# Performance work log

Hardware: AMD Instinct MI355X
Metric: run time of the kernel (lower is better)

## Reference

```python
import jax, jax.numpy as jnp
import numpy as np
from jax import lax

B, C, L = 32, 8, 4096
K, S = 128, 64  # num_shapelets, shapelets_size


def setup_inputs() -> dict:
    key = jax.random.key(0)
    kx, ks = jax.random.split(key)
    x = jax.random.normal(kx, (B, C, L), dtype=jnp.float32)
    shapelets = jax.random.normal(ks, (C, K, S), dtype=jnp.float32)
    return {"x": x, "shapelets": shapelets}


def reference(x, shapelets):
    # x: (B, C, L); shapelets: (C, K, S)
    # Equivalent to: unfold -> cdist(p=2) -> sum over channels -> min over windows.
    # Use the ||a-b||^2 = ||a||^2 + ||b||^2 - 2 a.b expansion so the unfolded
    # (B, C, W, S) tensor is never materialized; cross-terms via grouped conv.
    Bc, Cc, Lc = x.shape
    _, Kc, Sc = shapelets.shape
    dn = ("NCH", "OIH", "NCH")
    # cross[b, c*K+k, w] = sum_s x[b,c,w+s] * shapelets[c,k,s]
    rhs = shapelets.reshape(Cc * Kc, 1, Sc)
    cross = lax.conv_general_dilated(x, rhs, (1,), "VALID",
                                     feature_group_count=Cc,
                                     dimension_numbers=dn)  # (B, C*K, W)
    W = cross.shape[-1]
    cross = cross.reshape(Bc, Cc, Kc, W)
    # sliding window squared norms of x: conv of x^2 with ones kernel per channel
    ones = jnp.ones((Cc, 1, Sc), x.dtype)
    xnorm = lax.conv_general_dilated(x * x, ones, (1,), "VALID",
                                     feature_group_count=Cc,
                                     dimension_numbers=dn)  # (B, C, W)
    snorm = jnp.sum(shapelets * shapelets, axis=-1)  # (C, K)
    d2 = xnorm[:, :, None, :] + snorm[None, :, :, None] - 2.0 * cross  # (B,C,K,W)
    d = jnp.sqrt(jnp.maximum(d2, 1e-12))
    summed = jnp.sum(d, axis=1, keepdims=True)  # (B, 1, K, W)
    return jnp.min(summed, axis=3)  # (B, 1, K)
```

## Files before the change

kernel.cpp:

```cpp
#include <hip/hip_runtime.h>


typedef short short8 __attribute__((ext_vector_type(8)));
typedef float f32x4 __attribute__((ext_vector_type(4)));

constexpr int Bn = 32, Cn = 8, Ln = 4096, Kn = 128, Sn = 64;
constexpr int Wn = Ln - Sn + 1;
constexpr int WT = 128;
constexpr int NWT = (Wn + WT - 1) / WT;
constexpr int BDIM = 256;

__device__ __forceinline__ unsigned int f2bf(float f) {
  unsigned int u = __float_as_uint(f);
  u += 0x7FFFu + ((u >> 16) & 1u);
  return u >> 16;
}

__global__ void prep_kernel(const float* __restrict__ sh,
                            unsigned int* __restrict__ out,
                            unsigned short* __restrict__ hbf,
                            float* __restrict__ snorm) {
  int gid = blockIdx.x * blockDim.x + threadIdx.x;
  out[gid] = 0x7F7FFFFFu;
  if (gid < Cn * Kn) {
    const float4* row = (const float4*)(sh + (size_t)gid * Sn);
    uint2* orow = (uint2*)(hbf + (size_t)gid * Sn);
    float a = 0.f;
    #pragma unroll
    for (int i = 0; i < 16; ++i) {
      float4 v = row[i];
      a += v.x * v.x + v.y * v.y + v.z * v.z + v.w * v.w;
      unsigned int p0 = f2bf(-2.f * v.x) | (f2bf(-2.f * v.y) << 16);
      unsigned int p1 = f2bf(-2.f * v.z) | (f2bf(-2.f * v.w) << 16);
      orow[i] = make_uint2(p0, p1);
    }
    snorm[gid] = a;
  }
}

__launch_bounds__(BDIM, 2)
__global__ void med_kernel(const float* __restrict__ x,
                           const unsigned short* __restrict__ hbf,
                           const float* __restrict__ snorm,
                           unsigned int* __restrict__ out) {
  constexpr int XRS = 200;
  constexpr int BSS = 80;
  __shared__ __align__(16) unsigned short Xr[8 * XRS];
  __shared__ __align__(16) unsigned short Bs[Kn * BSS];
  __shared__ __align__(16) float xnormC[Cn * WT];
  __shared__ __align__(16) float snormC[Cn * Kn];

  const int tid  = threadIdx.x;
  const int b    = blockIdx.y;
  const int w0   = blockIdx.x * WT;
  const int lane = tid & 63;
  const int wv   = tid >> 6;
  const int quad = lane >> 4;
  const int n16  = lane & 15;
  const int wbase = wv * 32;

  const float* xb = x + (size_t)b * Cn * Ln;

  ((float4*)snormC)[tid] = ((const float4*)snorm)[tid];

  {
    int c  = tid >> 5;
    int m0 = (tid & 31) * 4;
    const float* xc = xb + c * Ln;
    auto xq = [&](int i) -> float {
      float v = (i < Ln) ? xc[i] : 0.f;
      return v * v;
    };
    float s0 = 0.f;
    for (int s = 0; s < Sn; ++s) s0 += xq(w0 + m0 + s);
    float s1 = s0 - xq(w0 + m0 + 0) + xq(w0 + m0 + 64);
    float s2 = s1 - xq(w0 + m0 + 1) + xq(w0 + m0 + 65);
    float s3 = s2 - xq(w0 + m0 + 2) + xq(w0 + m0 + 66);
    xnormC[c * WT + m0 + 0] = s0;
    xnormC[c * WT + m0 + 1] = s1;
    xnormC[c * WT + m0 + 2] = s2;
    xnormC[c * WT + m0 + 3] = s3;
  }

  float dist[2][8][4] = {};

  for (int c = 0; c < Cn; ++c) {
    __syncthreads();

    {
      const float* xc = xb + c * Ln;
      #pragma unroll
      for (int rep = 0; rep < 3; ++rep) {
        int pid = tid + rep * BDIM;
        int r = pid / 96;
        int p = pid - r * 96;
        int i0 = w0 + r + 2 * p;
        float f0 = (i0 < Ln) ? xc[i0] : 0.f;
        float f1 = (i0 + 1 < Ln) ? xc[i0 + 1] : 0.f;
        *(unsigned int*)(&Xr[r * XRS + 2 * p]) = f2bf(f0) | (f2bf(f1) << 16);
      }
    }
    {
      const uint4* hb = (const uint4*)(hbf + (size_t)c * Kn * Sn);
      #pragma unroll
      for (int rep = 0; rep < 4; ++rep) {
        int qid = tid + rep * BDIM;
        int k = qid >> 3, ch = qid & 7;
        *(uint4*)(&Bs[k * BSS + ch * 8]) = hb[qid];
      }
    }
    __syncthreads();

    float4 xn[2];
    #pragma unroll
    for (int mt = 0; mt < 2; ++mt)
      xn[mt] = *(const float4*)(&xnormC[c * WT + wbase + mt * 16 + quad * 4]);

    short8 af[2][2];
    #pragma unroll
    for (int mt = 0; mt < 2; ++mt)
      #pragma unroll
      for (int ks = 0; ks < 2; ++ks) {
        int i = wbase + mt * 16 + n16 + ks * 32 + quad * 8;
        af[mt][ks] = *(const short8*)(&Xr[(i & 7) * XRS + (i >> 3) * 8]);
      }

    #pragma unroll
    for (int pass = 0; pass < 2; ++pass) {
      short8 bfr[4][2];
      float sn[4];
      #pragma unroll
      for (int nt = 0; nt < 4; ++nt) {
        int ksh = pass * 64 + nt * 16 + n16;
        sn[nt] = snormC[c * Kn + ksh];
        #pragma unroll
        for (int ks = 0; ks < 2; ++ks)
          bfr[nt][ks] = *(const short8*)(&Bs[ksh * BSS + ks * 32 + quad * 8]);
      }
      #pragma unroll
      for (int mt = 0; mt < 2; ++mt)
        #pragma unroll
        for (int nt = 0; nt < 4; ++nt) {
          f32x4 acc;
          #pragma unroll
          for (int rg = 0; rg < 4; ++rg) acc[rg] = xn[mt][rg] + sn[nt];
          acc = __builtin_amdgcn_mfma_f32_16x16x32_bf16(af[mt][0], bfr[nt][0], acc, 0, 0, 0);
          acc = __builtin_amdgcn_mfma_f32_16x16x32_bf16(af[mt][1], bfr[nt][1], acc, 0, 0, 0);
          #pragma unroll
          for (int rg = 0; rg < 4; ++rg)
            dist[mt][pass * 4 + nt][rg] += __builtin_amdgcn_sqrtf(acc[rg]);
        }
    }
  }

  const int wql = w0 + wbase + quad * 4;
  #pragma unroll
  for (int nt2 = 0; nt2 < 8; ++nt2) {
    float v = 3.4e38f;
    #pragma unroll
    for (int mt = 0; mt < 2; ++mt)
      #pragma unroll
      for (int rg = 0; rg < 4; ++rg) {
        int wg = wql + mt * 16 + rg;
        float d = (wg < Wn) ? dist[mt][nt2][rg] : 3.4e38f;
        v = fminf(v, d);
      }
    v = fminf(v, __shfl_xor(v, 16, 64));
    v = fminf(v, __shfl_xor(v, 32, 64));
    if (lane < 16)
      atomicMin(&out[b * Kn + nt2 * 16 + n16], __float_as_uint(v));
  }
}

extern "C" void kernel_launch(void* const* d_in, const int* in_sizes, int n_in,
                              void* d_out, int out_size, void* d_ws, size_t ws_size,
                              hipStream_t stream) {
  const float* x  = (const float*)d_in[0];
  const float* sh = (const float*)d_in[1];
  unsigned int* out = (unsigned int*)d_out;
  unsigned short* hbf = (unsigned short*)d_ws;
  float* snorm = (float*)((char*)d_ws + (size_t)Cn * Kn * Sn * 2);
  hipLaunchKernelGGL(prep_kernel, dim3(16), dim3(256), 0, stream, sh, out, hbf, snorm);
  hipLaunchKernelGGL(med_kernel, dim3(NWT, Bn), dim3(BDIM), 0, stream, x, hbf, snorm, out);
}
```

Baseline: 112.8 us.

## Double-buffer channel staging with async global-to-LDS loads and XOR-swizzled B

Double-buffers the per-channel x tile and shapelet tile in shared memory. The next channel's data is prefetched while the current channel's MFMAs run: shapelets are copied directly global-to-LDS via global_load_lds, and x values are held in registers and written after compute. The shapelet layout is XOR-swizzled in the prep kernel so the unpadded LDS rows avoid bank conflicts, and launch bounds ask for 3 blocks per SM. The aim is to hide load latency and cut one barrier per channel, at the cost of more LDS and register pressure.

```diff
diff --git a/kernel.cpp b/kernel.cpp
--- a/kernel.cpp
+++ b/kernel.cpp
@@ -9,6 +9,9 @@
 constexpr int WT = 128;
 constexpr int NWT = (Wn + WT - 1) / WT;
 constexpr int BDIM = 256;
+
+typedef const __attribute__((address_space(1))) unsigned int gas_u32;
+typedef __attribute__((address_space(3))) unsigned int las_u32;
 
 __device__ __forceinline__ unsigned int f2bf(float f) {
   unsigned int u = __float_as_uint(f);
@@ -24,7 +27,8 @@
   out[gid] = 0x7F7FFFFFu;
   if (gid < Cn * Kn) {
     const float4* row = (const float4*)(sh + (size_t)gid * Sn);
-    uint2* orow = (uint2*)(hbf + (size_t)gid * Sn);
+    char* rowb = (char*)hbf + (size_t)gid * (Sn * 2);
+    const unsigned int sw = (gid & 7u) << 4;
     float a = 0.f;
     #pragma unroll
     for (int i = 0; i < 16; ++i) {
@@ -32,21 +36,20 @@
       a += v.x * v.x + v.y * v.y + v.z * v.z + v.w * v.w;
       unsigned int p0 = f2bf(-2.f * v.x) | (f2bf(-2.f * v.y) << 16);
       unsigned int p1 = f2bf(-2.f * v.z) | (f2bf(-2.f * v.w) << 16);
-      orow[i] = make_uint2(p0, p1);
+      *(uint2*)(rowb + ((8u * i) ^ sw)) = make_uint2(p0, p1);
     }
     snorm[gid] = a;
   }
 }
 
-__launch_bounds__(BDIM, 2)
+__launch_bounds__(BDIM, 3)
 __global__ void med_kernel(const float* __restrict__ x,
                            const unsigned short* __restrict__ hbf,
                            const float* __restrict__ snorm,
                            unsigned int* __restrict__ out) {
   constexpr int XRS = 200;
-  constexpr int BSS = 80;
-  __shared__ __align__(16) unsigned short Xr[8 * XRS];
-  __shared__ __align__(16) unsigned short Bs[Kn * BSS];
+  __shared__ __align__(16) unsigned short Xr[2][8 * XRS];
+  __shared__ __align__(16) unsigned short Bs[2][Kn * Sn];
   __shared__ __align__(16) float xnormC[Cn * WT];
   __shared__ __align__(16) float snormC[Cn * Kn];
 
@@ -61,7 +64,47 @@
 
   const float* xb = x + (size_t)b * Cn * Ln;
 
+  auto stage_b = [&](int bufi, int c) {
+    const char* src = (const char*)hbf + (size_t)c * (Kn * Sn * 2);
+    char* dst = (char*)&Bs[bufi][0];
+    #pragma unroll
+    for (int rep = 0; rep < 4; ++rep) {
+      int q16 = (tid + rep * BDIM) * 16;
+      __builtin_amdgcn_global_load_lds((gas_u32*)(src + q16), (las_u32*)(dst + q16),
+                                       16, 0, 0);
+    }
+  };
+
+  int x_lds[3], x_g[3];
+  #pragma unroll
+  for (int rep = 0; rep < 3; ++rep) {
+    int pid = tid + rep * BDIM;
+    int r = pid / 96;
+    int p = pid - r * 96;
+    x_lds[rep] = r * XRS + 2 * p;
+    x_g[rep] = w0 + r + 2 * p;
+  }
+  float xf[3][2];
+  auto load_x = [&](int c) {
+    const float* xc = xb + (size_t)c * Ln;
+    #pragma unroll
+    for (int rep = 0; rep < 3; ++rep) {
+      int i0 = x_g[rep];
+      xf[rep][0] = (i0 < Ln) ? xc[i0] : 0.f;
+      xf[rep][1] = (i0 + 1 < Ln) ? xc[i0 + 1] : 0.f;
+    }
+  };
+  auto write_x = [&](int bufi) {
+    #pragma unroll
+    for (int rep = 0; rep < 3; ++rep)
+      *(unsigned int*)(&Xr[bufi][x_lds[rep]]) =
+          f2bf(xf[rep][0]) | (f2bf(xf[rep][1]) << 16);
+  };
+
   ((float4*)snormC)[tid] = ((const float4*)snorm)[tid];
+
+  stage_b(0, 0);
+  load_x(0);
 
   {
     int c  = tid >> 5;
@@ -81,35 +124,18 @@
     xnormC[c * WT + m0 + 2] = s2;
     xnormC[c * WT + m0 + 3] = s3;
   }
+  write_x(0);
+  __syncthreads();
 
   float dist[2][8][4] = {};
 
   for (int c = 0; c < Cn; ++c) {
-    __syncthreads();
-
-    {
-      const float* xc = xb + c * Ln;
-      #pragma unroll
-      for (int rep = 0; rep < 3; ++rep) {
-        int pid = tid + rep * BDIM;
-        int r = pid / 96;
-        int p = pid - r * 96;
-        int i0 = w0 + r + 2 * p;
-        float f0 = (i0 < Ln) ? xc[i0] : 0.f;
-        float f1 = (i0 + 1 < Ln) ? xc[i0 + 1] : 0.f;
-        *(unsigned int*)(&Xr[r * XRS + 2 * p]) = f2bf(f0) | (f2bf(f1) << 16);
-      }
-    }
-    {
-      const uint4* hb = (const uint4*)(hbf + (size_t)c * Kn * Sn);
-      #pragma unroll
-      for (int rep = 0; rep < 4; ++rep) {
-        int qid = tid + rep * BDIM;
-        int k = qid >> 3, ch = qid & 7;
-        *(uint4*)(&Bs[k * BSS + ch * 8]) = hb[qid];
-      }
-    }
-    __syncthreads();
+    const int buf = c & 1;
+
+    if (c + 1 < Cn) {
+      stage_b(buf ^ 1, c + 1);
+      load_x(c + 1);
+    }
 
     float4 xn[2];
     #pragma unroll
@@ -122,9 +148,10 @@
       #pragma unroll
       for (int ks = 0; ks < 2; ++ks) {
         int i = wbase + mt * 16 + n16 + ks * 32 + quad * 8;
-        af[mt][ks] = *(const short8*)(&Xr[(i & 7) * XRS + (i >> 3) * 8]);
+        af[mt][ks] = *(const short8*)(&Xr[buf][(i & 7) * XRS + (i >> 3) * 8]);
       }
 
+    const char* bsb = (const char*)&Bs[buf][0];
     #pragma unroll
     for (int pass = 0; pass < 2; ++pass) {
       short8 bfr[4][2];
@@ -134,8 +161,10 @@
         int ksh = pass * 64 + nt * 16 + n16;
         sn[nt] = snormC[c * Kn + ksh];
         #pragma unroll
-        for (int ks = 0; ks < 2; ++ks)
-          bfr[nt][ks] = *(const short8*)(&Bs[ksh * BSS + ks * 32 + quad * 8]);
+        for (int ks = 0; ks < 2; ++ks) {
+          int off = (ksh * 128 + ks * 64 + quad * 16) ^ ((ksh & 7) << 4);
+          bfr[nt][ks] = *(const short8*)(bsb + off);
+        }
       }
       #pragma unroll
       for (int mt = 0; mt < 2; ++mt)
@@ -151,6 +180,9 @@
             dist[mt][pass * 4 + nt][rg] += __builtin_amdgcn_sqrtf(acc[rg]);
         }
     }
+
+    if (c + 1 < Cn) write_x(buf ^ 1);
+    __syncthreads();
   }
 
   const int wql = w0 + wbase + quad * 4;
```

Measured after the change: 205.3 us. 1.82x slower.

## Stage all channels of x in LDS once and read shapelets directly from global

Applied to the files above, without the earlier changes.

The kernel now converts the x tile for all eight channels to bf16 in shared memory up front, with a single barrier, instead of reloading per channel between two barriers. Shapelet B-fragments and norms are loaded straight from global/L2 into registers, which removes the Bs and snormC staging. The K dimension is split into two halves of 64 in a non-unrolled outer loop, so the dist accumulators shrink and register pressure drops. The tradeoffs are redundant global loads of shapelets, since every wave reads them, and shapelet loads that are no longer amortised through LDS.

```diff
diff --git a/kernel.cpp b/kernel.cpp
--- a/kernel.cpp
+++ b/kernel.cpp
@@ -44,11 +44,8 @@
                            const float* __restrict__ snorm,
                            unsigned int* __restrict__ out) {
   constexpr int XRS = 200;
-  constexpr int BSS = 80;
-  __shared__ __align__(16) unsigned short Xr[8 * XRS];
-  __shared__ __align__(16) unsigned short Bs[Kn * BSS];
+  __shared__ __align__(16) unsigned short Xr[Cn][8 * XRS];
   __shared__ __align__(16) float xnormC[Cn * WT];
-  __shared__ __align__(16) float snormC[Cn * Kn];
 
   const int tid  = threadIdx.x;
   const int b    = blockIdx.y;
@@ -61,7 +58,32 @@
 
   const float* xb = x + (size_t)b * Cn * Ln;
 
-  ((float4*)snormC)[tid] = ((const float4*)snorm)[tid];
+  int x_lds[3], x_g[3];
+  #pragma unroll
+  for (int rep = 0; rep < 3; ++rep) {
+    int pid = tid + rep * BDIM;
+    int r = pid / 96;
+    int p = pid - r * 96;
+    x_lds[rep] = r * XRS + 2 * p;
+    x_g[rep] = w0 + r + 2 * p;
+  }
+  const bool safe = (w0 + 198 <= Ln);
+  #pragma unroll 1
+  for (int c = 0; c < Cn; ++c) {
+    const float* xc = xb + (size_t)c * Ln;
+    #pragma unroll
+    for (int rep = 0; rep < 3; ++rep) {
+      float f0, f1;
+      if (safe) {
+        f0 = xc[x_g[rep]];
+        f1 = xc[x_g[rep] + 1];
+      } else {
+        f0 = (x_g[rep] < Ln) ? xc[x_g[rep]] : 0.f;
+        f1 = (x_g[rep] + 1 < Ln) ? xc[x_g[rep] + 1] : 0.f;
+      }
+      *(unsigned int*)(&Xr[c][x_lds[rep]]) = f2bf(f0) | (f2bf(f1) << 16);
+    }
+  }
 
   {
     int c  = tid >> 5;
@@ -71,8 +93,14 @@
       float v = (i < Ln) ? xc[i] : 0.f;
       return v * v;
     };
-    float s0 = 0.f;
-    for (int s = 0; s < Sn; ++s) s0 += xq(w0 + m0 + s);
+    float a0 = 0.f, a1 = 0.f, a2 = 0.f, a3 = 0.f;
+    for (int s = 0; s < Sn; s += 4) {
+      a0 += xq(w0 + m0 + s);
+      a1 += xq(w0 + m0 + s + 1);
+      a2 += xq(w0 + m0 + s + 2);
+      a3 += xq(w0 + m0 + s + 3);
+    }
+    float s0 = (a0 + a1) + (a2 + a3);
     float s1 = s0 - xq(w0 + m0 + 0) + xq(w0 + m0 + 64);
     float s2 = s1 - xq(w0 + m0 + 1) + xq(w0 + m0 + 65);
     float s3 = s2 - xq(w0 + m0 + 2) + xq(w0 + m0 + 66);
@@ -81,94 +109,68 @@
     xnormC[c * WT + m0 + 2] = s2;
     xnormC[c * WT + m0 + 3] = s3;
   }
+  __syncthreads();
 
-  float dist[2][8][4] = {};
+  const int wql = w0 + wbase + quad * 4;
+  const char* hbase = (const char*)hbf + n16 * 128 + quad * 16;
 
-  for (int c = 0; c < Cn; ++c) {
-    __syncthreads();
+  #pragma unroll 1
+  for (int gh = 0; gh < 2; ++gh) {
+    float dist[4][2][4] = {};
 
-    {
-      const float* xc = xb + c * Ln;
-      #pragma unroll
-      for (int rep = 0; rep < 3; ++rep) {
-        int pid = tid + rep * BDIM;
-        int r = pid / 96;
-        int p = pid - r * 96;
-        int i0 = w0 + r + 2 * p;
-        float f0 = (i0 < Ln) ? xc[i0] : 0.f;
-        float f1 = (i0 + 1 < Ln) ? xc[i0 + 1] : 0.f;
-        *(unsigned int*)(&Xr[r * XRS + 2 * p]) = f2bf(f0) | (f2bf(f1) << 16);
-      }
-    }
-    {
-      const uint4* hb = (const uint4*)(hbf + (size_t)c * Kn * Sn);
-      #pragma unroll
-      for (int rep = 0; rep < 4; ++rep) {
-        int qid = tid + rep * BDIM;
-        int k = qid >> 3, ch = qid & 7;
-        *(uint4*)(&Bs[k * BSS + ch * 8]) = hb[qid];
-      }
-    }
-    __syncthreads();
-
-    float4 xn[2];
-    #pragma unroll
-    for (int mt = 0; mt < 2; ++mt)
-      xn[mt] = *(const float4*)(&xnormC[c * WT + wbase + mt * 16 + quad * 4]);
-
-    short8 af[2][2];
-    #pragma unroll
-    for (int mt = 0; mt < 2; ++mt)
-      #pragma unroll
-      for (int ks = 0; ks < 2; ++ks) {
-        int i = wbase + mt * 16 + n16 + ks * 32 + quad * 8;
-        af[mt][ks] = *(const short8*)(&Xr[(i & 7) * XRS + (i >> 3) * 8]);
-      }
-
-    #pragma unroll
-    for (int pass = 0; pass < 2; ++pass) {
-      short8 bfr[4][2];
-      float sn[4];
-      #pragma unroll
-      for (int nt = 0; nt < 4; ++nt) {
-        int ksh = pass * 64 + nt * 16 + n16;
-        sn[nt] = snormC[c * Kn + ksh];
-        #pragma unroll
-        for (int ks = 0; ks < 2; ++ks)
-          bfr[nt][ks] = *(const short8*)(&Bs[ksh * BSS + ks * 32 + quad * 8]);
-      }
+    #pragma unroll 1
+    for (int c = 0; c < Cn; ++c) {
+      short8 af[2][2];
       #pragma unroll
       for (int mt = 0; mt < 2; ++mt)
         #pragma unroll
-        for (int nt = 0; nt < 4; ++nt) {
+        for (int ks = 0; ks < 2; ++ks) {
+          int i = wbase + mt * 16 + n16 + ks * 32 + quad * 8;
+          af[mt][ks] = *(const short8*)(&Xr[c][(i & 7) * XRS + (i >> 3) * 8]);
+        }
+      float4 xn[2];
+      #pragma unroll
+      for (int mt = 0; mt < 2; ++mt)
+        xn[mt] = *(const float4*)(&xnormC[c * WT + wbase + mt * 16 + quad * 4]);
+
+      const char* hc = hbase + (c * Kn + gh * 64) * (Sn * 2);
+      const float* snc = snorm + c * Kn + gh * 64 + n16;
+
+      #pragma unroll
+      for (int gl = 0; gl < 4; ++gl) {
+        short8 b0 = *(const short8*)(hc + gl * 2048);
+        short8 b1 = *(const short8*)(hc + gl * 2048 + 64);
+        float sn = snc[gl * 16];
+        #pragma unroll
+        for (int mt = 0; mt < 2; ++mt) {
           f32x4 acc;
           #pragma unroll
-          for (int rg = 0; rg < 4; ++rg) acc[rg] = xn[mt][rg] + sn[nt];
-          acc = __builtin_amdgcn_mfma_f32_16x16x32_bf16(af[mt][0], bfr[nt][0], acc, 0, 0, 0);
-          acc = __builtin_amdgcn_mfma_f32_16x16x32_bf16(af[mt][1], bfr[nt][1], acc, 0, 0, 0);
+          for (int rg = 0; rg < 4; ++rg) acc[rg] = xn[mt][rg] + sn;
+          acc = __builtin_amdgcn_mfma_f32_16x16x32_bf16(af[mt][0], b0, acc, 0, 0, 0);
+          acc = __builtin_amdgcn_mfma_f32_16x16x32_bf16(af[mt][1], b1, acc, 0, 0, 0);
           #pragma unroll
           for (int rg = 0; rg < 4; ++rg)
-            dist[mt][pass * 4 + nt][rg] += __builtin_amdgcn_sqrtf(acc[rg]);
+            dist[gl][mt][rg] += __builtin_amdgcn_sqrtf(acc[rg]);
         }
+      }
     }
-  }
 
-  const int wql = w0 + wbase + quad * 4;
-  #pragma unroll
-  for (int nt2 = 0; nt2 < 8; ++nt2) {
-    float v = 3.4e38f;
     #pragma unroll
-    for (int mt = 0; mt < 2; ++mt)
+    for (int gl = 0; gl < 4; ++gl) {
+      float v = 3.4e38f;
       #pragma unroll
-      for (int rg = 0; rg < 4; ++rg) {
-        int wg = wql + mt * 16 + rg;
-        float d = (wg < Wn) ? dist[mt][nt2][rg] : 3.4e38f;
-        v = fminf(v, d);
-      }
-    v = fminf(v, __shfl_xor(v, 16, 64));
-    v = fminf(v, __shfl_xor(v, 32, 64));
-    if (lane < 16)
-      atomicMin(&out[b * Kn + nt2 * 16 + n16], __float_as_uint(v));
+      for (int mt = 0; mt < 2; ++mt)
+        #pragma unroll
+        for (int rg = 0; rg < 4; ++rg) {
+          int wg = wql + mt * 16 + rg;
+          float d = (wg < Wn) ? dist[gl][mt][rg] : 3.4e38f;
+          v = fminf(v, d);
+        }
+      v = fminf(v, __shfl_xor(v, 16, 64));
+      v = fminf(v, __shfl_xor(v, 32, 64));
+      if (lane < 16)
+        atomicMin(&out[b * Kn + (gh * 4 + gl) * 16 + n16], __float_as_uint(v));
+    }
   }
 }
 
```

Result: slower. 141.3 us (+25.2%).

## Split shapelets across waves, double-buffer per-wave LDS staging, drop block barriers

Applied to the files above, without the earlier changes.

Each wave now owns a 32-shapelet slice across all 128 windows instead of a 32-window slice across all shapelets, so every wave stages its own B tile (via global_load_lds into XOR-swizzled LDS) and its own copy of the bf16 window tile. This removes the per-channel __syncthreads and lets the next channel's loads be issued before the current channel's MFMAs, a double-buffered software pipeline. The cost is that each wave redundantly converts and stores the whole X tile, which means more global loads and LDS traffic. LDS use also grows, which may lower occupancy.

```diff
diff --git a/kernel.cpp b/kernel.cpp
--- a/kernel.cpp
+++ b/kernel.cpp
@@ -9,6 +9,12 @@
 constexpr int WT = 128;
 constexpr int NWT = (Wn + WT - 1) / WT;
 constexpr int BDIM = 256;
+constexpr int XRS = 200;
+constexpr int PPR = 96;
+constexpr int PAIRS = 8 * PPR;
+
+typedef const __attribute__((address_space(1))) unsigned int gas_u32;
+typedef __attribute__((address_space(3))) unsigned int las_u32;
 
 __device__ __forceinline__ unsigned int f2bf(float f) {
   unsigned int u = __float_as_uint(f);
@@ -24,7 +30,8 @@
   out[gid] = 0x7F7FFFFFu;
   if (gid < Cn * Kn) {
     const float4* row = (const float4*)(sh + (size_t)gid * Sn);
-    uint2* orow = (uint2*)(hbf + (size_t)gid * Sn);
+    char* rowb = (char*)hbf + (size_t)gid * (Sn * 2);
+    const unsigned int sw = (gid & 7u) << 4;
     float a = 0.f;
     #pragma unroll
     for (int i = 0; i < 16; ++i) {
@@ -32,7 +39,7 @@
       a += v.x * v.x + v.y * v.y + v.z * v.z + v.w * v.w;
       unsigned int p0 = f2bf(-2.f * v.x) | (f2bf(-2.f * v.y) << 16);
       unsigned int p1 = f2bf(-2.f * v.z) | (f2bf(-2.f * v.w) << 16);
-      orow[i] = make_uint2(p0, p1);
+      *(uint2*)(rowb + ((8u * i) ^ sw)) = make_uint2(p0, p1);
     }
     snorm[gid] = a;
   }
@@ -43,10 +50,8 @@
                            const unsigned short* __restrict__ hbf,
                            const float* __restrict__ snorm,
                            unsigned int* __restrict__ out) {
-  constexpr int XRS = 200;
-  constexpr int BSS = 80;
-  __shared__ __align__(16) unsigned short Xr[8 * XRS];
-  __shared__ __align__(16) unsigned short Bs[Kn * BSS];
+  __shared__ __align__(16) unsigned short Xr[4][2][8 * XRS];
+  __shared__ __align__(16) unsigned short Bs[4][32 * Sn];
   __shared__ __align__(16) float xnormC[Cn * WT];
   __shared__ __align__(16) float snormC[Cn * Kn];
 
@@ -57,11 +62,48 @@
   const int wv   = tid >> 6;
   const int quad = lane >> 4;
   const int n16  = lane & 15;
-  const int wbase = wv * 32;
+  const int kq   = wv;
 
   const float* xb = x + (size_t)b * Cn * Ln;
 
+  auto stage_b = [&](int c) {
+    const char* src = (const char*)hbf + ((size_t)c * Kn + kq * 32) * (Sn * 2);
+    char* dst = (char*)&Bs[wv][0];
+    #pragma unroll
+    for (int rep = 0; rep < 4; ++rep) {
+      int q16 = lane * 16 + rep * 1024;
+      __builtin_amdgcn_global_load_lds((gas_u32*)(src + q16), (las_u32*)(dst + q16),
+                                       16, 0, 0);
+    }
+  };
+
+  auto stage_x = [&](int c, int xbuf) {
+    const float* xc = xb + (size_t)c * Ln;
+    #pragma unroll
+    for (int bt = 0; bt < 3; ++bt) {
+      float a[4][2];
+      #pragma unroll
+      for (int sub = 0; sub < 4; ++sub) {
+        int pid = lane + (bt * 4 + sub) * 64;
+        int r = pid / PPR, p = pid - r * PPR;
+        int i0 = w0 + r + 2 * p;
+        a[sub][0] = (i0 < Ln) ? xc[i0] : 0.f;
+        a[sub][1] = (i0 + 1 < Ln) ? xc[i0 + 1] : 0.f;
+      }
+      #pragma unroll
+      for (int sub = 0; sub < 4; ++sub) {
+        int pid = lane + (bt * 4 + sub) * 64;
+        int r = pid / PPR, p = pid - r * PPR;
+        *(unsigned int*)(&Xr[wv][xbuf][r * XRS + 2 * p]) =
+            f2bf(a[sub][0]) | (f2bf(a[sub][1]) << 16);
+      }
+    }
+  };
+
   ((float4*)snormC)[tid] = ((const float4*)snorm)[tid];
+
+  stage_b(0);
+  stage_x(0, 0);
 
   {
     int c  = tid >> 5;
@@ -81,94 +123,70 @@
     xnormC[c * WT + m0 + 2] = s2;
     xnormC[c * WT + m0 + 3] = s3;
   }
-
-  float dist[2][8][4] = {};
+  __syncthreads();
+
+  float dist[8][2][4] = {};
+  int buf = 0;
 
   for (int c = 0; c < Cn; ++c) {
-    __syncthreads();
-
-    {
-      const float* xc = xb + c * Ln;
-      #pragma unroll
-      for (int rep = 0; rep < 3; ++rep) {
-        int pid = tid + rep * BDIM;
-        int r = pid / 96;
-        int p = pid - r * 96;
-        int i0 = w0 + r + 2 * p;
-        float f0 = (i0 < Ln) ? xc[i0] : 0.f;
-        float f1 = (i0 + 1 < Ln) ? xc[i0 + 1] : 0.f;
-        *(unsigned int*)(&Xr[r * XRS + 2 * p]) = f2bf(f0) | (f2bf(f1) << 16);
-      }
-    }
-    {
-      const uint4* hb = (const uint4*)(hbf + (size_t)c * Kn * Sn);
-      #pragma unroll
-      for (int rep = 0; rep < 4; ++rep) {
-        int qid = tid + rep * BDIM;
-        int k = qid >> 3, ch = qid & 7;
-        *(uint4*)(&Bs[k * BSS + ch * 8]) = hb[qid];
-      }
-    }
-    __syncthreads();
-
-    float4 xn[2];
-    #pragma unroll
-    for (int mt = 0; mt < 2; ++mt)
-      xn[mt] = *(const float4*)(&xnormC[c * WT + wbase + mt * 16 + quad * 4]);
-
-    short8 af[2][2];
-    #pragma unroll
-    for (int mt = 0; mt < 2; ++mt)
-      #pragma unroll
-      for (int ks = 0; ks < 2; ++ks) {
-        int i = wbase + mt * 16 + n16 + ks * 32 + quad * 8;
-        af[mt][ks] = *(const short8*)(&Xr[(i & 7) * XRS + (i >> 3) * 8]);
-      }
-
-    #pragma unroll
-    for (int pass = 0; pass < 2; ++pass) {
-      short8 bfr[4][2];
-      float sn[4];
-      #pragma unroll
-      for (int nt = 0; nt < 4; ++nt) {
-        int ksh = pass * 64 + nt * 16 + n16;
-        sn[nt] = snormC[c * Kn + ksh];
+    asm volatile("s_waitcnt vmcnt(0)" ::: "memory");
+
+    short8 bq[2][2];
+    const char* bsb = (const char*)&Bs[wv][0];
+    #pragma unroll
+    for (int nt = 0; nt < 2; ++nt) {
+      int rl = nt * 16 + n16;
+      int boff = (rl * 128 + quad * 16) ^ ((rl & 7) << 4);
+      bq[nt][0] = *(const short8*)(bsb + boff);
+      bq[nt][1] = *(const short8*)(bsb + (boff ^ 64));
+    }
+    float sn0 = snormC[c * Kn + kq * 32 + n16];
+    float sn1 = snormC[c * Kn + kq * 32 + 16 + n16];
+
+    asm volatile("s_waitcnt lgkmcnt(0)" ::: "memory");
+    if (c + 1 < Cn) {
+      stage_b(c + 1);
+      stage_x(c + 1, buf ^ 1);
+    }
+
+    #pragma unroll
+    for (int mt = 0; mt < 8; ++mt) {
+      float4 xn = *(const float4*)(&xnormC[c * WT + mt * 16 + quad * 4]);
+      int i0 = mt * 16 + n16 + quad * 8;
+      short8 a0 = *(const short8*)(&Xr[wv][buf][(i0 & 7) * XRS + (i0 >> 3) * 8]);
+      int i1 = i0 + 32;
+      short8 a1 = *(const short8*)(&Xr[wv][buf][(i1 & 7) * XRS + (i1 >> 3) * 8]);
+      #pragma unroll
+      for (int nt = 0; nt < 2; ++nt) {
+        float sn = nt ? sn1 : sn0;
+        f32x4 acc;
         #pragma unroll
-        for (int ks = 0; ks < 2; ++ks)
-          bfr[nt][ks] = *(const short8*)(&Bs[ksh * BSS + ks * 32 + quad * 8]);
-      }
-      #pragma unroll
-      for (int mt = 0; mt < 2; ++mt)
+        for (int rg = 0; rg < 4; ++rg) acc[rg] = xn[rg] + sn;
+        acc = __builtin_amdgcn_mfma_f32_16x16x32_bf16(a0, bq[nt][0], acc, 0, 0, 0);
+        acc = __builtin_amdgcn_mfma_f32_16x16x32_bf16(a1, bq[nt][1], acc, 0, 0, 0);
         #pragma unroll
-        for (int nt = 0; nt < 4; ++nt) {
-          f32x4 acc;
-          #pragma unroll
-          for (int rg = 0; rg < 4; ++rg) acc[rg] = xn[mt][rg] + sn[nt];
-          acc = __builtin_amdgcn_mfma_f32_16x16x32_bf16(af[mt][0], bfr[nt][0], acc, 0, 0, 0);
-          acc = __builtin_amdgcn_mfma_f32_16x16x32_bf16(af[mt][1], bfr[nt][1], acc, 0, 0, 0);
-          #pragma unroll
-          for (int rg = 0; rg < 4; ++rg)
-            dist[mt][pass * 4 + nt][rg] += __builtin_amdgcn_sqrtf(acc[rg]);
-        }
-    }
-  }
-
-  const int wql = w0 + wbase + quad * 4;
+        for (int rg = 0; rg < 4; ++rg)
+          dist[mt][nt][rg] += __builtin_amdgcn_sqrtf(acc[rg]);
+      }
+    }
+    buf ^= 1;
+  }
+
   #pragma unroll
-  for (int nt2 = 0; nt2 < 8; ++nt2) {
+  for (int nt = 0; nt < 2; ++nt) {
     float v = 3.4e38f;
     #pragma unroll
-    for (int mt = 0; mt < 2; ++mt)
+    for (int mt = 0; mt < 8; ++mt)
       #pragma unroll
       for (int rg = 0; rg < 4; ++rg) {
-        int wg = wql + mt * 16 + rg;
-        float d = (wg < Wn) ? dist[mt][nt2][rg] : 3.4e38f;
+        int wg = w0 + mt * 16 + quad * 4 + rg;
+        float d = (wg < Wn) ? dist[mt][nt][rg] : 3.4e38f;
         v = fminf(v, d);
       }
     v = fminf(v, __shfl_xor(v, 16, 64));
     v = fminf(v, __shfl_xor(v, 32, 64));
     if (lane < 16)
-      atomicMin(&out[b * Kn + nt2 * 16 + n16], __float_as_uint(v));
+      atomicMin(&out[b * Kn + kq * 32 + nt * 16 + n16], __float_as_uint(v));
   }
 }
 
```

New measurement: 121.7 us. +7.8%, slower.
